# Kernel tuning notes

Measured on AMD Instinct MI355X. Metric: run time of the kernel, lower is better.

The kernel has to match this reference:

```python
import jax, jax.numpy as jnp
import numpy as np

B, N, H = 8, 512, 256
D2 = H // 2          # per-direction hidden = attention proj = 128
VOCAB, EMB = 100, 256
DIN0 = EMB + 3


def _sru_pp_layer(x, pad, Wq, Wk, Wv, Wu, vf, vr, bf, br):
    # x: (L, Bt, din); pad: (L, Bt) bool, True = padded position
    L, Bt, _ = x.shape
    d2 = Wu.shape[1] // 8
    q = x @ Wq                                   # (L,Bt,proj) attention projection
    k = q @ Wk
    v = q @ Wv
    scale = 1.0 / jnp.sqrt(jnp.asarray(q.shape[-1], q.dtype))
    scores = jnp.einsum('lbp,mbp->blm', q, k) * scale
    scores = jnp.where(pad.T[:, None, :], -1e9, scores)
    a = jnp.einsum('blm,mbp->lbp', jax.nn.softmax(scores, axis=-1), v) + q
    U = (a @ Wu).reshape(L, Bt, 2, 4, d2)        # 2 directions x 4 matrices

    def run_dir(Ud, padd, vf_d, vr_d, bf_d, br_d):
        def step(c, inp):
            u, p = inp                            # u: (Bt,4,d2), p: (Bt,)
            f = jax.nn.sigmoid(u[:, 1] + vf_d * c + bf_d)
            r = jax.nn.sigmoid(u[:, 2] + vr_d * c + br_d)
            c_new = f * c + (1.0 - f) * u[:, 0]
            c_new = jnp.where(p[:, None], c, c_new)
            h = jnp.where(p[:, None], 0.0, r * c_new + (1.0 - r) * u[:, 3])
            return c_new, h
        c0 = jnp.zeros((Bt, d2), x.dtype)
        _, hs = jax.lax.scan(step, c0, (Ud, padd))
        return hs

    hf = run_dir(U[:, :, 0], pad, vf[0], vr[0], bf[0], br[0])
    hb = run_dir(U[::-1, :, 1], pad[::-1], vf[1], vr[1], bf[1], br[1])[::-1]
    return jnp.concatenate([hf, hb], axis=-1)     # (L,Bt,2*d2)


def _forward(noisy_seqs, noisy_cords, mask, emb, params):
    Bb, Nn = noisy_seqs.shape
    X = noisy_cords[:, :, 1]                      # CA coordinates (B,N,3)
    m3 = mask[..., None]
    center = (X * m3).sum(1) / m3.sum(1)
    Xc = X - center[:, None] * m3
    C = jnp.einsum('bni,bnj->bij', Xc, Xc)        # (B,3,3) covariance
    _, V = jnp.linalg.eigh(jax.lax.stop_gradient(C))
    ops = jnp.asarray([[i, j, k] for i in (-1, 1) for j in (-1, 1) for k in (-1, 1)], X.dtype)
    F_ops = ops[None, :, None, :] * V[:, None]    # (B,8,3,3) sign-flipped frames
    hX = jnp.einsum('boji,bpj->bopi', F_ops, Xc).reshape(Bb * 8, Nn, 3)
    seq = jnp.where(noisy_seqs < 0, 82, noisy_seqs)
    hS = jnp.broadcast_to(emb[seq][:, None], (Bb, 8, Nn, emb.shape[1])).reshape(Bb * 8, Nn, -1)
    h = jnp.swapaxes(jnp.concatenate([hX, hS], -1), 0, 1)   # (N, B*8, EMB+3)
    pad = jnp.broadcast_to((mask == 0.0)[:, None], (Bb, 8, Nn)).reshape(Bb * 8, Nn).T
    for p in params:
        h = _sru_pp_layer(h, pad, *p)
    return jnp.swapaxes(h, 0, 1).reshape(Bb, 8, Nn, -1).mean(1)


def setup_inputs():
    key = jax.random.key(0)
    ks = [jax.random.fold_in(key, i) for i in range(32)]
    inp = {
        'noisy_seqs': jax.random.randint(ks[0], (B, N), 0, VOCAB, dtype=jnp.int32),
        'noisy_cords': jax.random.normal(ks[1], (B, N, 4, 3), jnp.float32),
        'mask': jnp.ones((B, N), jnp.float32),
        'emb': 0.02 * jax.random.normal(ks[2], (VOCAB, EMB), jnp.float32),
    }
    i = 3
    for l, din in enumerate([DIN0, H]):
        inp[f'Wq{l}'] = jax.random.normal(ks[i], (din, D2), jnp.float32) / np.sqrt(din); i += 1
        inp[f'Wk{l}'] = jax.random.normal(ks[i], (D2, D2), jnp.float32) / np.sqrt(D2); i += 1
        inp[f'Wv{l}'] = jax.random.normal(ks[i], (D2, D2), jnp.float32) / np.sqrt(D2); i += 1
        inp[f'Wu{l}'] = jax.random.normal(ks[i], (D2, 8 * D2), jnp.float32) / np.sqrt(D2); i += 1
        inp[f'vf{l}'] = 0.1 * jax.random.normal(ks[i], (2, D2), jnp.float32); i += 1
        inp[f'vr{l}'] = 0.1 * jax.random.normal(ks[i], (2, D2), jnp.float32); i += 1
        inp[f'bf{l}'] = jnp.zeros((2, D2), jnp.float32)
        inp[f'br{l}'] = jnp.zeros((2, D2), jnp.float32)
    return inp


def reference(noisy_seqs, noisy_cords, mask, emb,
              Wq0, Wk0, Wv0, Wu0, vf0, vr0, bf0, br0,
              Wq1, Wk1, Wv1, Wu1, vf1, vr1, bf1, br1):
    params = [(Wq0, Wk0, Wv0, Wu0, vf0, vr0, bf0, br0),
              (Wq1, Wk1, Wv1, Wu1, vf1, vr1, bf1, br1)]
    return _forward(noisy_seqs, noisy_cords, mask, emb, params)
```

## Files before the change

### kernel.cpp

```cpp
#include <hip/hip_runtime.h>
#include <hip/hip_bf16.h>
#include <math.h>

#define L_    512
#define F_    64
#define M_    (F_*L_)
#define D2_   128
#define H_    256
#define LOG2E_ 1.4426950408889634f

typedef unsigned short u16;
typedef __attribute__((ext_vector_type(8))) short s16x8;
typedef __attribute__((ext_vector_type(4))) float f32x4;

__device__ inline u16 bf_hi(float x) {
  union { float f; unsigned u; } v; v.f = x;
  unsigned r = v.u + 0x7fffu + ((v.u >> 16) & 1u);
  return (u16)(r >> 16);
}
__device__ inline float bf_to_f(u16 h) {
  union { float f; unsigned u; } v; v.u = ((unsigned)h) << 16; return v.f;
}
__device__ inline void split2(float x, u16& h, u16& l) {
  h = bf_hi(x);
  l = bf_hi(x - bf_to_f(h));
}
__device__ inline float exp2_fast(float x) {
#if __has_builtin(__builtin_amdgcn_exp2f)
  return __builtin_amdgcn_exp2f(x);
#else
  return __expf(x * 0.6931471805599453f);
#endif
}
__device__ inline float rcp_fast(float x) {
#if __has_builtin(__builtin_amdgcn_rcpf)
  return __builtin_amdgcn_rcpf(x);
#else
  return 1.f/x;
#endif
}

#define RSPLIT_A 18432
#define RSPLIT_B 26624

__global__ void geom_kernel(const float* __restrict__ cords, const float* __restrict__ mask,
                            float* __restrict__ misc) {
  int b = blockIdx.x;
  int t = threadIdx.x;
  __shared__ float red[4][256];
  float sx=0.f, sy=0.f, sz=0.f, sm=0.f;
  for (int l = t; l < 512; l += 256) {
    float m = mask[b*512 + l];
    const float* X = cords + ((size_t)(b*512 + l)*4 + 1)*3;
    sx += X[0]*m; sy += X[1]*m; sz += X[2]*m; sm += m;
  }
  red[0][t]=sx; red[1][t]=sy; red[2][t]=sz; red[3][t]=sm;
  __syncthreads();
  for (int off=128; off>0; off>>=1) {
    if (t < off) { red[0][t]+=red[0][t+off]; red[1][t]+=red[1][t+off];
                   red[2][t]+=red[2][t+off]; red[3][t]+=red[3][t+off]; }
    __syncthreads();
  }
  float inv = 1.f/red[3][0];
  float cx = red[0][0]*inv, cy = red[1][0]*inv, cz = red[2][0]*inv;
  __syncthreads();
  __shared__ float red6[6][256];
  float c00=0,c01=0,c02=0,c11=0,c12=0,c22=0;
  for (int l = t; l < 512; l += 256) {
    float m = mask[b*512+l];
    const float* X = cords + ((size_t)(b*512+l)*4 + 1)*3;
    float x = X[0]-cx*m, y = X[1]-cy*m, z = X[2]-cz*m;
    c00+=x*x; c01+=x*y; c02+=x*z; c11+=y*y; c12+=y*z; c22+=z*z;
  }
  red6[0][t]=c00; red6[1][t]=c01; red6[2][t]=c02;
  red6[3][t]=c11; red6[4][t]=c12; red6[5][t]=c22;
  __syncthreads();
  for (int off=128; off>0; off>>=1) {
    if (t < off) for (int j=0;j<6;j++) red6[j][t]+=red6[j][t+off];
    __syncthreads();
  }
  if (t == 0) {
    double A[3][3], V[3][3];
    A[0][0]=red6[0][0]; A[0][1]=A[1][0]=red6[1][0]; A[0][2]=A[2][0]=red6[2][0];
    A[1][1]=red6[3][0]; A[1][2]=A[2][1]=red6[4][0]; A[2][2]=red6[5][0];
    for (int j=0;j<3;j++) for (int i=0;i<3;i++) V[j][i] = (i==j)?1.0:0.0;
    for (int sweep=0; sweep<10; ++sweep) {
      for (int p=0;p<2;p++) for (int q=p+1;q<3;q++) {
        double apq = A[p][q];
        if (fabs(apq) < 1e-18) continue;
        double app = A[p][p], aqq = A[q][q];
        double tau = (aqq - app) / (2.0*apq);
        double tt = (tau >= 0.0) ? 1.0/(tau + sqrt(1.0+tau*tau))
                                 : 1.0/(tau - sqrt(1.0+tau*tau));
        double cc = 1.0/sqrt(1.0+tt*tt), ss = tt*cc;
        A[p][p] = app - tt*apq;
        A[q][q] = aqq + tt*apq;
        A[p][q] = A[q][p] = 0.0;
        int r = 3 - p - q;
        double arp = A[r][p], arq = A[r][q];
        A[r][p] = A[p][r] = cc*arp - ss*arq;
        A[r][q] = A[q][r] = ss*arp + cc*arq;
        for (int rr2=0; rr2<3; ++rr2) {
          double vrp = V[rr2][p], vrq = V[rr2][q];
          V[rr2][p] = cc*vrp - ss*vrq;
          V[rr2][q] = ss*vrp + cc*vrq;
        }
      }
    }
    double w[3] = {A[0][0], A[1][1], A[2][2]};
    int idx[3] = {0,1,2};
    for (int i=0;i<2;i++) for (int j=0;j<2-i;j++)
      if (w[idx[j]] > w[idx[j+1]]) { int tmp=idx[j]; idx[j]=idx[j+1]; idx[j+1]=tmp; }
    for (int jj=0;jj<3;jj++) for (int ii=0;ii<3;ii++)
      misc[b*12 + jj*3 + ii] = (float)V[jj][idx[ii]];
    misc[b*12+9]=cx; misc[b*12+10]=cy; misc[b*12+11]=cz;
  }
}

__global__ void build_h0(const int* __restrict__ seqs, const float* __restrict__ cords,
                         const float* __restrict__ mask, const float* __restrict__ emb,
                         const float* __restrict__ misc,
                         u16* __restrict__ h0h, u16* __restrict__ h0l) {
  int t = threadIdx.x;
  int r = blockIdx.x*4 + (t >> 6);
  int lane = t & 63;
  int f = r >> 9, l = r & 511;
  int b = f >> 3, o = f & 7;
  u16* rh = h0h + (size_t)r * 288;
  u16* rl = h0l + (size_t)r * 288;
  if (lane == 0) {
    float m = mask[b*512 + l];
    const float* X = cords + ((size_t)(b*512 + l)*4 + 1)*3;
    const float* mb = misc + b*12;
    float x = X[0]-mb[9]*m, y = X[1]-mb[10]*m, z = X[2]-mb[11]*m;
    #pragma unroll
    for (int i=0;i<3;i++) {
      float sgn = ((o >> (2-i)) & 1) ? 1.f : -1.f;
      float val = sgn * (mb[0+i]*x + mb[3+i]*y + mb[6+i]*z);
      u16 h,lo; split2(val,h,lo); rh[i]=h; rl[i]=lo;
    }
  }
  if (lane < 29) { rh[259+lane] = 0; rl[259+lane] = 0; }
  int s = seqs[b*512 + l];
  if (s < 0) s = 82;
  const float4 e4 = *((const float4*)(emb + (size_t)s*256) + lane);
  float ev[4] = {e4.x, e4.y, e4.z, e4.w};
  #pragma unroll
  for (int i=0;i<4;i++) {
    u16 h,lo; split2(ev[i],h,lo);
    rh[3 + lane*4 + i] = h; rl[3 + lane*4 + i] = lo;
  }
}

__global__ void prep_wqkv_mul(const float* __restrict__ Wq, const float* __restrict__ Wk,
                              const float* __restrict__ Wv,
                              float* __restrict__ wqk, float* __restrict__ wqv) {
  int k = blockIdx.x;
  int y = blockIdx.y;
  int t = threadIdx.x;
  __shared__ float row[128];
  row[t] = Wq[(size_t)k*128 + t];
  __syncthreads();
  const float* W2 = y ? Wv : Wk;
  float acc = 0.f;
  for (int j = 0; j < 128; j++) acc += row[j] * W2[(size_t)j*128 + t];
  (y ? wqv : wqk)[(size_t)k*128 + t] = acc;
}

__global__ void prep_wT3(const float* __restrict__ Wq, const float* __restrict__ wqk,
                         const float* __restrict__ wqv,
                         u16* __restrict__ Th, u16* __restrict__ Tl,
                         int K, int KP) {
  int y = blockIdx.y;
  int n = blockIdx.x;
  const float* W = (y==0) ? Wq : (y==1) ? wqk : wqv;
  int row = y*128 + n;
  for (int k = threadIdx.x; k < KP; k += 128) {
    float x = (k < K) ? W[(size_t)k*128 + n] : 0.f;
    u16 h,l; split2(x,h,l);
    Th[(size_t)row*KP + k] = h; Tl[(size_t)row*KP + k] = l;
  }
}

__global__ void prep_wu(const float* __restrict__ Wu, u16* __restrict__ Th, u16* __restrict__ Tl,
                        const float* __restrict__ bfv, const float* __restrict__ brv,
                        float* __restrict__ nbf, float* __restrict__ nbr) {
  int n = blockIdx.x;
  int dir = blockIdx.y;
  int k = threadIdx.x;
  int d = n >> 2, g = n & 3;
  float x = Wu[(size_t)k*1024 + (dir*4+g)*128 + d];
  if (g == 1 || g == 2) x *= -LOG2E_;
  u16 h,l; split2(x,h,l);
  size_t o = ((size_t)dir*512 + n)*128 + k;
  Th[o]=h; Tl[o]=l;
  if (n == 0) {
    nbf[dir*128 + k] = bfv[dir*128 + k] * (-LOG2E_);
    nbr[dir*128 + k] = brv[dir*128 + k] * (-LOG2E_);
  }
}

__global__ __launch_bounds__(256) void gemm_qkv(
    const u16* __restrict__ Ah, const u16* __restrict__ Al,
    const u16* __restrict__ Bh, const u16* __restrict__ Bl,
    int KP,
    u16* __restrict__ Ch, u16* __restrict__ Cl,
    u16* __restrict__ Dh, u16* __restrict__ Dl,
    u16* __restrict__ Eh, u16* __restrict__ El)
{
  __shared__ u16 As[2][64][40];
  __shared__ u16 Bs[2][128][40];
  const int t = threadIdx.x;
  const int bm = blockIdx.x * 64, bn = blockIdx.y * 128;
  const int lane = t & 63;
  const int w = t >> 6;
  const int fr = lane & 15, g = lane >> 4;

  f32x4 acc[4][2] = {};

  for (int k0 = 0; k0 < KP; k0 += 32) {
    {
      int m = t >> 2, sub = t & 3;
      const size_t ga = (size_t)(bm + m)*KP + k0 + sub*8;
      *(int4*)&As[0][m][sub*8] = *(const int4*)(Ah + ga);
      *(int4*)&As[1][m][sub*8] = *(const int4*)(Al + ga);
    }
    #pragma unroll
    for (int cc = 0; cc < 2; cc++) {
      int c = t + cc*256;
      int m = c >> 2, sub = c & 3;
      const size_t gb = (size_t)(bn + m)*KP + k0 + sub*8;
      *(int4*)&Bs[0][m][sub*8] = *(const int4*)(Bh + gb);
      *(int4*)&Bs[1][m][sub*8] = *(const int4*)(Bl + gb);
    }
    __syncthreads();
    s16x8 af[4][2], bfr[2][2];
    #pragma unroll
    for (int i = 0; i < 4; i++) {
      af[i][0] = *(const s16x8*)&As[0][i*16 + fr][g*8];
      af[i][1] = *(const s16x8*)&As[1][i*16 + fr][g*8];
    }
    #pragma unroll
    for (int j = 0; j < 2; j++) {
      bfr[j][0] = *(const s16x8*)&Bs[0][w*32 + j*16 + fr][g*8];
      bfr[j][1] = *(const s16x8*)&Bs[1][w*32 + j*16 + fr][g*8];
    }
    #pragma unroll
    for (int mi = 0; mi < 4; mi++)
      #pragma unroll
      for (int nj = 0; nj < 2; nj++)
        acc[mi][nj] = __builtin_amdgcn_mfma_f32_16x16x32_bf16(af[mi][0], bfr[nj][0], acc[mi][nj], 0,0,0);
    #pragma unroll
    for (int mi = 0; mi < 4; mi++)
      #pragma unroll
      for (int nj = 0; nj < 2; nj++)
        acc[mi][nj] = __builtin_amdgcn_mfma_f32_16x16x32_bf16(af[mi][0], bfr[nj][1], acc[mi][nj], 0,0,0);
    #pragma unroll
    for (int mi = 0; mi < 4; mi++)
      #pragma unroll
      for (int nj = 0; nj < 2; nj++)
        acc[mi][nj] = __builtin_amdgcn_mfma_f32_16x16x32_bf16(af[mi][1], bfr[nj][0], acc[mi][nj], 0,0,0);
    __syncthreads();
  }

  #pragma unroll
  for (int mi = 0; mi < 4; mi++) {
    #pragma unroll
    for (int nj = 0; nj < 2; nj++) {
      #pragma unroll
      for (int rg = 0; rg < 4; rg++) {
        int r = bm + mi*16 + g*4 + rg;
        int n = bn + w*32 + nj*16 + fr;
        float val = acc[mi][nj][rg];
        u16 h,l; split2(val,h,l);
        if (blockIdx.y == 0) {
          size_t o = (size_t)r*128 + n;
          Ch[o]=h; Cl[o]=l;
        } else if (blockIdx.y == 1) {
          size_t o = (size_t)r*128 + (n - 128);
          Dh[o]=h; Dl[o]=l;
        } else {
          size_t o = ((size_t)(r >> 9)*128 + (n - 256))*512 + (r & 511);
          Eh[o]=h; El[o]=l;
        }
      }
    }
  }
}

template<int EPI>
__global__ __launch_bounds__(256) void gemm_bb(
    const u16* __restrict__ Ah, const u16* __restrict__ Al,
    const u16* __restrict__ Bh, const u16* __restrict__ Bl,
    int KP, int lda, int ldb,
    long aBatch, long bBatch, long cBatch,
    u16* __restrict__ Ch, u16* __restrict__ Cl, int ldc,
    float* __restrict__ F0, float* __restrict__ F1, float* __restrict__ F2,
    float* __restrict__ F3, float* __restrict__ F4, float* __restrict__ F5,
    const u16* __restrict__ rh, const u16* __restrict__ rl,
    const float* __restrict__ maskp, const float* __restrict__ nbf,
    const float* __restrict__ nbr, float scale, int dirOff)
{
  __shared__ u16 As[2][128][40];
  __shared__ u16 Bs[2][128][40];
  __shared__ float epsM[128];
  __shared__ float epsA[128];
  const int t = threadIdx.x;
  const int z = blockIdx.z;
  const int bm = blockIdx.x * 128, bn = blockIdx.y * 128;
  Ah += (size_t)z * aBatch; Al += (size_t)z * aBatch;
  Bh += (size_t)z * bBatch; Bl += (size_t)z * bBatch;

  const int lane = t & 63;
  const int w = t >> 6, wr = w >> 1, wc = w & 1;
  const int fr = lane & 15, g = lane >> 4;

  const bool isD1 = (bn >= 512);
  const int dirU = dirOff + (isD1 ? 1 : 0);
  if (EPI == 4) {
    if (t < 128) {
      int r = bm + t;
      epsM[t] = maskp[(r >> 12)*512 + (r & 511)];
      int nl = (bn + t) & 511;
      int dd = nl >> 2, gg2 = nl & 3;
      epsA[t] = (gg2==1) ? nbf[dirU*128 + dd] : (gg2==2) ? nbr[dirU*128 + dd] : 0.f;
    }
  }

  f32x4 acc[4][4] = {};

  for (int k0 = 0; k0 < KP; k0 += 32) {
    #pragma unroll
    for (int cc = 0; cc < 2; cc++) {
      int c = t + cc*256;
      int m = c >> 2, sub = c & 3;
      const size_t ga = (size_t)(bm + m)*lda + k0 + sub*8;
      const size_t gb = (size_t)(bn + m)*ldb + k0 + sub*8;
      *(int4*)&As[0][m][sub*8] = *(const int4*)(Ah + ga);
      *(int4*)&As[1][m][sub*8] = *(const int4*)(Al + ga);
      *(int4*)&Bs[0][m][sub*8] = *(const int4*)(Bh + gb);
      *(int4*)&Bs[1][m][sub*8] = *(const int4*)(Bl + gb);
    }
    __syncthreads();
    s16x8 af[4][2], bfr[4][2];
    #pragma unroll
    for (int i = 0; i < 4; i++) {
      af[i][0]  = *(const s16x8*)&As[0][wr*64 + i*16 + fr][g*8];
      af[i][1]  = *(const s16x8*)&As[1][wr*64 + i*16 + fr][g*8];
      bfr[i][0] = *(const s16x8*)&Bs[0][wc*64 + i*16 + fr][g*8];
      bfr[i][1] = *(const s16x8*)&Bs[1][wc*64 + i*16 + fr][g*8];
    }
    #pragma unroll
    for (int mi = 0; mi < 4; mi++)
      #pragma unroll
      for (int nj = 0; nj < 4; nj++)
        acc[mi][nj] = __builtin_amdgcn_mfma_f32_16x16x32_bf16(af[mi][0], bfr[nj][0], acc[mi][nj], 0,0,0);
    #pragma unroll
    for (int mi = 0; mi < 4; mi++)
      #pragma unroll
      for (int nj = 0; nj < 4; nj++)
        acc[mi][nj] = __builtin_amdgcn_mfma_f32_16x16x32_bf16(af[mi][0], bfr[nj][1], acc[mi][nj], 0,0,0);
    #pragma unroll
    for (int mi = 0; mi < 4; mi++)
      #pragma unroll
      for (int nj = 0; nj < 4; nj++)
        acc[mi][nj] = __builtin_amdgcn_mfma_f32_16x16x32_bf16(af[mi][1], bfr[nj][0], acc[mi][nj], 0,0,0);
    __syncthreads();
  }

  const int rbase = bm + wr*64, nbase = bn + wc*64;
  float* tA = isD1 ? F3 : F0;
  float* tB = isD1 ? F4 : F1;
  float* tC = isD1 ? F5 : F2;
  const int gg = fr & 3;
  const float ovr = (gg==1) ? -16384.f : (gg==2) ? 16384.f : 0.f;

  #pragma unroll
  for (int mi = 0; mi < 4; mi++) {
    #pragma unroll
    for (int nj = 0; nj < 4; nj++) {
      #pragma unroll
      for (int rg = 0; rg < 4; rg++) {
        int r = rbase + mi*16 + g*4 + rg;
        int n = nbase + nj*16 + fr;
        float val = acc[mi][nj][rg];
        if (EPI == 2) {
          float vv = val * scale;
          if (maskp[(z>>3)*512 + n] == 0.f) vv = -1e9f;
          F0[(size_t)z*cBatch + (size_t)r*ldc + n] = vv;
        } else if (EPI == 3) {
          size_t o = (size_t)z*cBatch + (size_t)r*ldc + n;
          float vv = val + (bf_to_f(rh[o]) + bf_to_f(rl[o]));
          u16 h,l; split2(vv,h,l);
          Ch[o]=h; Cl[o]=l;
        } else if (EPI == 4) {
          int nloc = (n & 511);
          val += epsA[n - bn];
          if (epsM[r - bm] == 0.f) val = ovr;
          float* Up;
          if (r < RSPLIT_A)      Up = tA + (size_t)r*512;
          else if (r < RSPLIT_B) Up = tB + (size_t)(r - RSPLIT_A)*512;
          else                   Up = tC + (size_t)(r - RSPLIT_B)*512;
          Up[nloc] = val;
        }
      }
    }
  }
}

__global__ __launch_bounds__(256) void attn_flash(
    const u16* __restrict__ qh, const u16* __restrict__ ql,
    const u16* __restrict__ kh, const u16* __restrict__ kl,
    const u16* __restrict__ vTh, const u16* __restrict__ vTl,
    const float* __restrict__ maskp,
    u16* __restrict__ ah, u16* __restrict__ al, float scale)
{
  __shared__ u16 As[2][64][36];
  __shared__ u16 Bs[2][128][36];
  __shared__ u16 Ps[2][64][68];
  __shared__ float rmaxL[2][64];
  __shared__ float rsumL[2][64];
  __shared__ float mskt[64];
  const int t = threadIdx.x;
  const int bid = blockIdx.x;
  const int xcd  = bid & 7;
  const int rest = bid >> 3;
  const int tile = rest & 7;
  const int f    = (rest >> 3)*8 + xcd;
  const int bq = f >> 3;
  const int bm = tile * 64;
  const size_t qrow0 = (size_t)f*512 + bm;
  const int lane = t & 63;
  const int w = t >> 6, wr = w >> 1, wc = w & 1;
  const int fr = lane & 15, g = lane >> 4;
  const int m_ = t >> 2, sub_ = t & 3;

  float mrun[2][4], srun[2][4];
  #pragma unroll
  for (int mi=0;mi<2;mi++)
    #pragma unroll
    for (int rg=0;rg<4;rg++) { mrun[mi][rg] = -3e38f; srun[mi][rg] = 0.f; }
  f32x4 Oacc[2][4] = {};

  for (int kt = 0; kt < 8; ++kt) {
    if (t < 64) mskt[t] = maskp[bq*512 + kt*64 + t];
    f32x4 Sacc[2][2] = {};
    #pragma unroll
    for (int k0 = 0; k0 < 4; ++k0) {
      {
        const size_t ga = (qrow0 + m_)*128 + k0*32 + sub_*8;
        const size_t gb = ((size_t)f*512 + kt*64 + m_)*128 + k0*32 + sub_*8;
        *(int4*)&As[0][m_][sub_*8] = *(const int4*)(qh + ga);
        *(int4*)&As[1][m_][sub_*8] = *(const int4*)(ql + ga);
        *(int4*)&Bs[0][m_][sub_*8] = *(const int4*)(kh + gb);
        *(int4*)&Bs[1][m_][sub_*8] = *(const int4*)(kl + gb);
      }
      __syncthreads();
      s16x8 af[2][2], bf2[2][2];
      #pragma unroll
      for (int i = 0; i < 2; i++) {
        af[i][0]  = *(const s16x8*)&As[0][wr*32 + i*16 + fr][g*8];
        af[i][1]  = *(const s16x8*)&As[1][wr*32 + i*16 + fr][g*8];
        bf2[i][0] = *(const s16x8*)&Bs[0][wc*32 + i*16 + fr][g*8];
        bf2[i][1] = *(const s16x8*)&Bs[1][wc*32 + i*16 + fr][g*8];
      }
      #pragma unroll
      for (int mi = 0; mi < 2; mi++)
        #pragma unroll
        for (int nj = 0; nj < 2; nj++)
          Sacc[mi][nj] = __builtin_amdgcn_mfma_f32_16x16x32_bf16(af[mi][0], bf2[nj][0], Sacc[mi][nj], 0,0,0);
      #pragma unroll
      for (int mi = 0; mi < 2; mi++)
        #pragma unroll
        for (int nj = 0; nj < 2; nj++)
          Sacc[mi][nj] = __builtin_amdgcn_mfma_f32_16x16x32_bf16(af[mi][0], bf2[nj][1], Sacc[mi][nj], 0,0,0);
      #pragma unroll
      for (int mi = 0; mi < 2; mi++)
        #pragma unroll
        for (int nj = 0; nj < 2; nj++)
          Sacc[mi][nj] = __builtin_amdgcn_mfma_f32_16x16x32_bf16(af[mi][1], bf2[nj][0], Sacc[mi][nj], 0,0,0);
      __syncthreads();
    }
    float mkv[2];
    mkv[0] = mskt[wc*32 + fr];
    mkv[1] = mskt[wc*32 + 16 + fr];
    float rm[2][4];
    #pragma unroll
    for (int mi=0;mi<2;mi++)
      #pragma unroll
      for (int rg=0;rg<4;rg++) rm[mi][rg] = -3e38f;
    #pragma unroll
    for (int mi=0;mi<2;mi++)
      #pragma unroll
      for (int nj=0;nj<2;nj++)
        #pragma unroll
        for (int rg=0;rg<4;rg++) {
          float sv = Sacc[mi][nj][rg]*scale;
          sv = (mkv[nj]==0.f) ? -1e9f : sv;
          Sacc[mi][nj][rg] = sv;
          rm[mi][rg] = fmaxf(rm[mi][rg], sv);
        }
    #pragma unroll
    for (int off=1; off<16; off<<=1)
      #pragma unroll
      for (int mi=0;mi<2;mi++)
        #pragma unroll
        for (int rg=0;rg<4;rg++) rm[mi][rg] = fmaxf(rm[mi][rg], __shfl_xor(rm[mi][rg], off));
    if (fr == 0) {
      #pragma unroll
      for (int mi=0;mi<2;mi++)
        #pragma unroll
        for (int rg=0;rg<4;rg++) rmaxL[wc][wr*32 + mi*16 + g*4 + rg] = rm[mi][rg];
    }
    __syncthreads();
    float alpha[2][4], rs[2][4];
    #pragma unroll
    for (int mi=0;mi<2;mi++)
      #pragma unroll
      for (int rg=0;rg<4;rg++) {
        int rl_ = wr*32 + mi*16 + g*4 + rg;
        float tmax = fmaxf(rmaxL[0][rl_], rmaxL[1][rl_]);
        float mn = fmaxf(mrun[mi][rg], tmax);
        alpha[mi][rg] = exp2_fast((mrun[mi][rg] - mn)*LOG2E_);
        mrun[mi][rg] = mn;
        rs[mi][rg] = 0.f;
      }
    #pragma unroll
    for (int mi=0;mi<2;mi++)
      #pragma unroll
      for (int nj=0;nj<2;nj++)
        #pragma unroll
        for (int rg=0;rg<4;rg++) {
          float p = exp2_fast((Sacc[mi][nj][rg] - mrun[mi][rg])*LOG2E_);
          rs[mi][rg] += p;
          u16 h,l; split2(p,h,l);
          int rl_ = wr*32 + mi*16 + g*4 + rg;
          int cl_ = wc*32 + nj*16 + fr;
          Ps[0][rl_][cl_] = h;
          Ps[1][rl_][cl_] = l;
        }
    #pragma unroll
    for (int off=1; off<16; off<<=1)
      #pragma unroll
      for (int mi=0;mi<2;mi++)
        #pragma unroll
        for (int rg=0;rg<4;rg++) rs[mi][rg] += __shfl_xor(rs[mi][rg], off);
    if (fr == 0) {
      #pragma unroll
      for (int mi=0;mi<2;mi++)
        #pragma unroll
        for (int rg=0;rg<4;rg++) rsumL[wc][wr*32 + mi*16 + g*4 + rg] = rs[mi][rg];
    }
    #pragma unroll
    for (int mi=0;mi<2;mi++)
      #pragma unroll
      for (int nj=0;nj<4;nj++)
        #pragma unroll
        for (int rg=0;rg<4;rg++) Oacc[mi][nj][rg] *= alpha[mi][rg];
    __syncthreads();
    #pragma unroll
    for (int mi=0;mi<2;mi++)
      #pragma unroll
      for (int rg=0;rg<4;rg++) {
        int rl_ = wr*32 + mi*16 + g*4 + rg;
        srun[mi][rg] = srun[mi][rg]*alpha[mi][rg] + rsumL[0][rl_] + rsumL[1][rl_];
      }
    #pragma unroll
    for (int k0 = 0; k0 < 2; ++k0) {
      #pragma unroll
      for (int cc = 0; cc < 2; cc++) {
        int c = t + cc*256;
        int mv = c >> 2, sb = c & 3;
        const size_t gv = ((size_t)f*128 + mv)*512 + kt*64 + k0*32 + sb*8;
        *(int4*)&Bs[0][mv][sb*8] = *(const int4*)(vTh + gv);
        *(int4*)&Bs[1][mv][sb*8] = *(const int4*)(vTl + gv);
      }
      __syncthreads();
      s16x8 pa[2][2], pb[4][2];
      #pragma unroll
      for (int i = 0; i < 2; i++) {
        pa[i][0] = *(const s16x8*)&Ps[0][wr*32 + i*16 + fr][k0*32 + g*8];
        pa[i][1] = *(const s16x8*)&Ps[1][wr*32 + i*16 + fr][k0*32 + g*8];
      }
      #pragma unroll
      for (int j = 0; j < 4; j++) {
        pb[j][0] = *(const s16x8*)&Bs[0][wc*64 + j*16 + fr][g*8];
        pb[j][1] = *(const s16x8*)&Bs[1][wc*64 + j*16 + fr][g*8];
      }
      #pragma unroll
      for (int mi = 0; mi < 2; mi++)
        #pragma unroll
        for (int nj = 0; nj < 4; nj++)
          Oacc[mi][nj] = __builtin_amdgcn_mfma_f32_16x16x32_bf16(pa[mi][0], pb[nj][0], Oacc[mi][nj], 0,0,0);
      #pragma unroll
      for (int mi = 0; mi < 2; mi++)
        #pragma unroll
        for (int nj = 0; nj < 4; nj++)
          Oacc[mi][nj] = __builtin_amdgcn_mfma_f32_16x16x32_bf16(pa[mi][0], pb[nj][1], Oacc[mi][nj], 0,0,0);
      #pragma unroll
      for (int mi = 0; mi < 2; mi++)
        #pragma unroll
        for (int nj = 0; nj < 4; nj++)
          Oacc[mi][nj] = __builtin_amdgcn_mfma_f32_16x16x32_bf16(pa[mi][1], pb[nj][0], Oacc[mi][nj], 0,0,0);
      __syncthreads();
    }
  }
  float inv[2][4];
  #pragma unroll
  for (int mi=0;mi<2;mi++)
    #pragma unroll
    for (int rg=0;rg<4;rg++) inv[mi][rg] = 1.f / srun[mi][rg];
  #pragma unroll
  for (int mi=0;mi<2;mi++)
    #pragma unroll
    for (int nj=0;nj<4;nj++)
      #pragma unroll
      for (int rg=0;rg<4;rg++) {
        int rl_ = wr*32 + mi*16 + g*4 + rg;
        int cl_ = wc*64 + nj*16 + fr;
        size_t o = (qrow0 + rl_)*128 + cl_;
        float val = Oacc[mi][nj][rg]*inv[mi][rg] + bf_to_f(qh[o]) + bf_to_f(ql[o]);
        u16 h,l; split2(val,h,l);
        ah[o]=h; al[o]=l;
      }
}

__global__ void softmax_split(float* __restrict__ S) {
  size_t row = blockIdx.x;
  float* p = S + row*512;
  u16* ph = (u16*)p;
  u16* pl = ph + 512;
  int t = threadIdx.x;
  float v[8];
  float mx = -1e30f;
  #pragma unroll
  for (int i=0;i<8;i++) { v[i] = p[t + i*64]; mx = fmaxf(mx, v[i]); }
  #pragma unroll
  for (int off=32; off>0; off>>=1) mx = fmaxf(mx, __shfl_xor(mx, off));
  float sum = 0.f;
  #pragma unroll
  for (int i=0;i<8;i++) { v[i] = __expf(v[i]-mx); sum += v[i]; }
  #pragma unroll
  for (int off=32; off>0; off>>=1) sum += __shfl_xor(sum, off);
  float invs = 1.f/sum;
  #pragma unroll
  for (int i=0;i<8;i++) {
    float x = v[i]*invs;
    u16 h,l; split2(x,h,l);
    ph[t + i*64] = h; pl[t + i*64] = l;
  }
}

#define CH_ 8
#define LOADC(buf, ch) do { \
  int _c = (ch); \
  _Pragma("unroll") \
  for (int s = 0; s < CH_; s++) { \
    int l = (_c*CH_ + s) ^ lxor; \
    buf[s] = *(const float4*)(Ubase + (size_t)l*512); \
  } \
  __builtin_amdgcn_sched_barrier(0); \
} while(0)

#define COMPC(buf, ch) do { \
  int _c = (ch); \
  _Pragma("unroll") \
  for (int s = 0; s < CH_; s++) { \
    int l = (_c*CH_ + s) ^ lxor; \
    float4 u = buf[s]; \
    float ef = exp2_fast(fmaf(nvfd, cstate, u.y)); \
    float fg = rcp_fast(1.f + ef); \
    float er = exp2_fast(fmaf(nvrd, cstate, u.z)); \
    float rg = rcp_fast(1.f + er); \
    float cn = fmaf(fg, cstate - u.x, u.x); \
    float h  = fmaf(rg, cn - u.w, u.w); \
    cstate = cn; \
    if (PAIRS) { \
      u16 sh_, sl_; split2(h, sh_, sl_); \
      hpph[(size_t)l*256] = sh_; \
      hppl[(size_t)l*256] = sl_; \
    } else { \
      h32p[(size_t)l*256] = h; \
    } \
  } \
  __builtin_amdgcn_sched_barrier(0); \
} while(0)

template<int PAIRS>
__global__ __launch_bounds__(64, 1) void sru_scan(
                          const float* __restrict__ ua0, const float* __restrict__ ub0,
                          const float* __restrict__ uc0,
                          const float* __restrict__ ua1, const float* __restrict__ ub1,
                          const float* __restrict__ uc1,
                          const float* __restrict__ vf, const float* __restrict__ vr,
                          u16* __restrict__ hph, u16* __restrict__ hpl,
                          float* __restrict__ h32, int dirArg) {
  const int blk = blockIdx.x;
  const int f = blk >> 1;
  const int hh = blk & 1;
  const int dir = dirArg + blockIdx.y;
  const int t = threadIdx.x;
  const int lxor = dir ? 511 : 0;
  const int d = hh*64 + t;
  const float nvfd = vf[dir*128 + d] * (-LOG2E_);
  const float nvrd = vr[dir*128 + d] * (-LOG2E_);
  const size_t fbase = (size_t)f * 512;
  const float* ua = dir ? ua1 : ua0;
  const float* ub = dir ? ub1 : ub0;
  const float* uc = dir ? uc1 : uc0;
  const float* Uf;
  if (f < 36)      Uf = ua + (size_t)f*(512*512);
  else if (f < 52) Uf = ub + (size_t)(f-36)*(512*512);
  else             Uf = uc + (size_t)(f-52)*(512*512);
  const float* Ubase = Uf + d*4;
  u16* hpph = hph + fbase*256 + (size_t)dir*128 + d;
  u16* hppl = hpl + fbase*256 + (size_t)dir*128 + d;
  float* h32p = h32 + fbase*256 + (size_t)dir*128 + d;

  float4 b0[CH_], b1[CH_], b2[CH_], b3[CH_];
  LOADC(b0, 0); LOADC(b1, 1);
  float cstate = 0.f;
  #pragma unroll 1
  for (int q4 = 0; q4 < 15; q4++) {
    const int base = q4*4;
    LOADC(b2, base+2);
    COMPC(b0, base);
    LOADC(b3, base+3);
    COMPC(b1, base+1);
    LOADC(b0, base+4);
    COMPC(b2, base+2);
    LOADC(b1, base+5);
    COMPC(b3, base+3);
  }
  LOADC(b2, 62);
  COMPC(b0, 60);
  LOADC(b3, 63);
  COMPC(b1, 61);
  COMPC(b2, 62);
  COMPC(b3, 63);
}

__global__ void mean_kernel(const float* __restrict__ h2, float* __restrict__ out) {
  int i = blockIdx.x*256 + threadIdx.x;
  int row = i >> 6;
  int c4  = i & 63;
  int b = row >> 9, l = row & 511;
  float ax=0.f, ay=0.f, az=0.f, aw=0.f;
  #pragma unroll
  for (int o=0;o<8;o++) {
    const float4* p = (const float4*)(h2 + ((size_t)((b*8+o)*512 + l))*256) + c4;
    float4 e = *p;
    ax += e.x; ay += e.y; az += e.z; aw += e.w;
  }
  float4 r; r.x = ax*0.125f; r.y = ay*0.125f; r.z = az*0.125f; r.w = aw*0.125f;
  ((float4*)out)[i] = r;
}

extern "C" void kernel_launch(void* const* d_in, const int* in_sizes, int n_in,
                              void* d_out, int out_size, void* d_ws, size_t ws_size,
                              hipStream_t stream) {
  const int*   seqs  = (const int*)d_in[0];
  const float* cords = (const float*)d_in[1];
  const float* mask  = (const float*)d_in[2];
  const float* emb   = (const float*)d_in[3];
  const float* Wq[2] = {(const float*)d_in[4],  (const float*)d_in[12]};
  const float* Wk[2] = {(const float*)d_in[5],  (const float*)d_in[13]};
  const float* Wv[2] = {(const float*)d_in[6],  (const float*)d_in[14]};
  const float* Wu[2] = {(const float*)d_in[7],  (const float*)d_in[15]};
  const float* vf[2] = {(const float*)d_in[8],  (const float*)d_in[16]};
  const float* vr[2] = {(const float*)d_in[9],  (const float*)d_in[17]};
  const float* bfp[2]= {(const float*)d_in[10], (const float*)d_in[18]};
  const float* brp[2]= {(const float*)d_in[11], (const float*)d_in[19]};

  const size_t H0_B = 2*(size_t)M_*288*2;
  const size_t Q_B  = 2*(size_t)M_*128*2;
  const size_t S_B  = (size_t)M_*512*4;
  const size_t HP_B = 2*(size_t)M_*256*2;
  const size_t W_B  = (size_t)(2*1024*128)*2 + 2*256*4;

  const size_t NEED_MERGED = 4096 + H0_B + 3*Q_B + S_B + HP_B + W_B;
  const bool merged = (ws_size >= NEED_MERGED);

  char* base = (char*)d_ws;
  float* misc = (float*)base;
  u16* h0p_h = (u16*)(base + 4096);
  u16* h0p_l = h0p_h + (size_t)M_*288;
  u16* q_h   = (u16*)(base + 4096 + H0_B);
  u16* q_l   = q_h + (size_t)M_*128;
  u16* k_h   = (u16*)(base + 4096 + H0_B + Q_B);
  u16* k_l   = k_h + (size_t)M_*128;

  u16 *vT_h, *vT_l, *a_h, *a_l;
  float *S, *tail_w;
  u16 *hp_h, *hp_l;
  float *U1A, *U1B, *U1C;
  if (merged) {
    vT_h = (u16*)(base + 4096 + H0_B + 2*Q_B);
    vT_l = vT_h + (size_t)M_*128;
    S    = (float*)(base + 4096 + H0_B + 3*Q_B);
    hp_h = (u16*)((char*)S + S_B);
    hp_l = hp_h + (size_t)M_*256;
    tail_w = (float*)((char*)hp_h + HP_B);
    U1A = (float*)h0p_h;
    U1B = (float*)q_h;
    U1C = (float*)vT_h;
    a_h = hp_h;
    a_l = hp_h + (size_t)M_*128;
  } else {
    S    = (float*)(base + 4096 + H0_B + 2*Q_B);
    hp_h = (u16*)((char*)S + S_B);
    hp_l = hp_h + (size_t)M_*256;
    vT_h = hp_h; vT_l = hp_l;
    tail_w = (float*)((char*)hp_h + HP_B);
    U1A = S; U1B = S + (size_t)RSPLIT_A*512; U1C = S + (size_t)RSPLIT_B*512;
    a_h = k_h; a_l = k_l;
  }
  float* U0A = S;
  float* U0B = S + (size_t)RSPLIT_A*512;
  float* U0C = S + (size_t)RSPLIT_B*512;
  float* h32 = (float*)hp_h;

  float* wqk32 = S;
  float* wqv32 = wqk32 + 288*128;
  u16*   wT3h  = (u16*)(wqv32 + 288*128);
  u16*   wT3l  = wT3h + 384*288;
  u16* wuT_h = (u16*)tail_w;
  u16* wuT_l = wuT_h + 1024*128;
  float* nbf = (float*)(wuT_l + 1024*128);
  float* nbr = nbf + 256;

  geom_kernel<<<8, 256, 0, stream>>>(cords, mask, misc);
  build_h0<<<M_/4, 256, 0, stream>>>(seqs, cords, mask, emb, misc, h0p_h, h0p_l);

  const float scale = 0.08838834764831845f;
  for (int layer = 0; layer < 2; ++layer) {
    const u16* Ah_in = layer ? hp_h : h0p_h;
    const u16* Al_in = layer ? hp_l : h0p_l;
    const int  Kq    = layer ? 256 : 259;
    const int  KPq   = layer ? 256 : 288;

    prep_wqkv_mul<<<dim3(Kq,2), 128, 0, stream>>>(Wq[layer], Wk[layer], Wv[layer], wqk32, wqv32);
    prep_wT3<<<dim3(128,3), 128, 0, stream>>>(Wq[layer], wqk32, wqv32, wT3h, wT3l, Kq, KPq);
    prep_wu<<<dim3(512,2), 128, 0, stream>>>(Wu[layer], wuT_h, wuT_l, bfp[layer], brp[layer], nbf, nbr);

    gemm_qkv<<<dim3(512,3), 256, 0, stream>>>(Ah_in, Al_in, wT3h, wT3l,
        KPq, q_h, q_l, k_h, k_l, vT_h, vT_l);

    if (merged) {
      attn_flash<<<512, 256, 0, stream>>>(q_h, q_l, k_h, k_l, vT_h, vT_l,
          mask, a_h, a_l, scale);
    } else {
      gemm_bb<2><<<dim3(4,4,64), 256, 0, stream>>>(q_h, q_l, k_h, k_l,
          128, 128, 128, 512*128, 512*128, 512*512, nullptr,nullptr, 512,
          S,nullptr,nullptr,nullptr,nullptr,nullptr,
          nullptr,nullptr, mask,nullptr,nullptr, scale, 0);
      softmax_split<<<M_, 64, 0, stream>>>(S);
      gemm_bb<3><<<dim3(4,1,64), 256, 0, stream>>>((const u16*)S, (const u16*)S + 512, vT_h, vT_l,
          512, 1024, 512, 512*1024, 128*512, 512*128, a_h, a_l, 128,
          nullptr,nullptr,nullptr,nullptr,nullptr,nullptr,
          q_h, q_l, nullptr,nullptr,nullptr, 0.f, 0);
    }

    if (merged) {
      gemm_bb<4><<<dim3(256,8,1), 256, 0, stream>>>(a_h, a_l, wuT_h, wuT_l,
          128, 128, 128, 0,0,0, nullptr,nullptr, 512,
          U0A,U0B,U0C, U1A,U1B,U1C,
          nullptr,nullptr, mask, nbf, nbr, 0.f, 0);
      if (layer == 0)
        sru_scan<1><<<dim3(128,2), 64, 0, stream>>>(U0A,U0B,U0C, U1A,U1B,U1C,
            vf[layer], vr[layer], hp_h, hp_l, h32, 0);
      else
        sru_scan<0><<<dim3(128,2), 64, 0, stream>>>(U0A,U0B,U0C, U1A,U1B,U1C,
            vf[layer], vr[layer], hp_h, hp_l, h32, 0);
    } else {
      for (int dir = 0; dir < 2; ++dir) {
        gemm_bb<4><<<dim3(256,4,1), 256, 0, stream>>>(a_h, a_l,
            wuT_h + (size_t)dir*512*128, wuT_l + (size_t)dir*512*128,
            128, 128, 128, 0,0,0, nullptr,nullptr, 512,
            U0A,U0B,U0C, U0A,U0B,U0C,
            nullptr,nullptr, mask, nbf, nbr, 0.f, dir);
        if (layer == 0)
          sru_scan<1><<<dim3(128,1), 64, 0, stream>>>(U0A,U0B,U0C, U0A,U0B,U0C,
              vf[layer], vr[layer], hp_h, hp_l, h32, dir);
        else
          sru_scan<0><<<dim3(128,1), 64, 0, stream>>>(U0A,U0B,U0C, U0A,U0B,U0C,
              vf[layer], vr[layer], hp_h, hp_l, h32, dir);
      }
    }
  }
  mean_kernel<<<1024, 256, 0, stream>>>(h32, (float*)d_out);
}
```

Measured before the change: 442.1 us.

## Halve flash-attention query tile to 32 rows and double block count

The flash attention kernel now handles 32 query rows per block instead of 64, so it launches 1024 blocks instead of 512. The four waves are re-split along the key/value column dimension, and the shared buffers are merged into one union buffer. The aim is more parallelism and better CU occupancy on the MI355X. In exchange, every K and V tile is loaded from global memory twice as often, and the row max/sum reduction now spans four waves.

```diff
diff --git a/kernel.cpp b/kernel.cpp
--- a/kernel.cpp
+++ b/kernel.cpp
@@ -415,91 +415,81 @@
     const float* __restrict__ maskp,
     u16* __restrict__ ah, u16* __restrict__ al, float scale)
 {
-  __shared__ u16 As[2][64][36];
-  __shared__ u16 Bs[2][128][36];
-  __shared__ u16 Ps[2][64][68];
-  __shared__ float rmaxL[2][64];
-  __shared__ float rsumL[2][64];
+  __shared__ __align__(16) u16 UB[9216];
+  __shared__ u16 Ps[2][32][68];
+  __shared__ float rmaxL[4][32];
+  __shared__ float rsumL[4][32];
   __shared__ float mskt[64];
   const int t = threadIdx.x;
   const int bid = blockIdx.x;
   const int xcd  = bid & 7;
   const int rest = bid >> 3;
-  const int tile = rest & 7;
-  const int f    = (rest >> 3)*8 + xcd;
+  const int tile = rest & 15;
+  const int f    = (rest >> 4)*8 + xcd;
   const int bq = f >> 3;
-  const int bm = tile * 64;
+  const int bm = tile * 32;
   const size_t qrow0 = (size_t)f*512 + bm;
   const int lane = t & 63;
-  const int w = t >> 6, wr = w >> 1, wc = w & 1;
+  const int w = t >> 6;
   const int fr = lane & 15, g = lane >> 4;
-  const int m_ = t >> 2, sub_ = t & 3;
 
   float mrun[2][4], srun[2][4];
   #pragma unroll
   for (int mi=0;mi<2;mi++)
     #pragma unroll
     for (int rg=0;rg<4;rg++) { mrun[mi][rg] = -3e38f; srun[mi][rg] = 0.f; }
-  f32x4 Oacc[2][4] = {};
+  f32x4 Oacc[2][2] = {};
 
   for (int kt = 0; kt < 8; ++kt) {
     if (t < 64) mskt[t] = maskp[bq*512 + kt*64 + t];
-    f32x4 Sacc[2][2] = {};
+    f32x4 Sacc[2] = {};
     #pragma unroll
     for (int k0 = 0; k0 < 4; ++k0) {
       {
-        const size_t ga = (qrow0 + m_)*128 + k0*32 + sub_*8;
-        const size_t gb = ((size_t)f*512 + kt*64 + m_)*128 + k0*32 + sub_*8;
-        *(int4*)&As[0][m_][sub_*8] = *(const int4*)(qh + ga);
-        *(int4*)&As[1][m_][sub_*8] = *(const int4*)(ql + ga);
-        *(int4*)&Bs[0][m_][sub_*8] = *(const int4*)(kh + gb);
-        *(int4*)&Bs[1][m_][sub_*8] = *(const int4*)(kl + gb);
+        int pl = t >> 7, id = t & 127, row = id >> 2, sub = id & 3;
+        const u16* src = pl ? ql : qh;
+        *(int4*)&UB[pl*1152 + row*36 + sub*8] =
+          *(const int4*)(src + (qrow0 + row)*128 + k0*32 + sub*8);
+      }
+      #pragma unroll
+      for (int cc = 0; cc < 2; cc++) {
+        int c = cc*256 + t;
+        int pl = c >> 8, id = c & 255, row = id >> 2, sub = id & 3;
+        const u16* src = pl ? kl : kh;
+        *(int4*)&UB[2304 + pl*2304 + row*36 + sub*8] =
+          *(const int4*)(src + ((size_t)f*512 + kt*64 + row)*128 + k0*32 + sub*8);
       }
       __syncthreads();
-      s16x8 af[2][2], bf2[2][2];
+      s16x8 af[2][2], bf2[2];
       #pragma unroll
       for (int i = 0; i < 2; i++) {
-        af[i][0]  = *(const s16x8*)&As[0][wr*32 + i*16 + fr][g*8];
-        af[i][1]  = *(const s16x8*)&As[1][wr*32 + i*16 + fr][g*8];
-        bf2[i][0] = *(const s16x8*)&Bs[0][wc*32 + i*16 + fr][g*8];
-        bf2[i][1] = *(const s16x8*)&Bs[1][wc*32 + i*16 + fr][g*8];
-      }
+        af[i][0] = *(const s16x8*)&UB[        (i*16 + fr)*36 + g*8];
+        af[i][1] = *(const s16x8*)&UB[1152 + (i*16 + fr)*36 + g*8];
+      }
+      bf2[0] = *(const s16x8*)&UB[2304 +        (w*16 + fr)*36 + g*8];
+      bf2[1] = *(const s16x8*)&UB[2304 + 2304 + (w*16 + fr)*36 + g*8];
       #pragma unroll
       for (int mi = 0; mi < 2; mi++)
-        #pragma unroll
-        for (int nj = 0; nj < 2; nj++)
-          Sacc[mi][nj] = __builtin_amdgcn_mfma_f32_16x16x32_bf16(af[mi][0], bf2[nj][0], Sacc[mi][nj], 0,0,0);
+        Sacc[mi] = __builtin_amdgcn_mfma_f32_16x16x32_bf16(af[mi][0], bf2[0], Sacc[mi], 0,0,0);
       #pragma unroll
       for (int mi = 0; mi < 2; mi++)
-        #pragma unroll
-        for (int nj = 0; nj < 2; nj++)
-          Sacc[mi][nj] = __builtin_amdgcn_mfma_f32_16x16x32_bf16(af[mi][0], bf2[nj][1], Sacc[mi][nj], 0,0,0);
+        Sacc[mi] = __builtin_amdgcn_mfma_f32_16x16x32_bf16(af[mi][0], bf2[1], Sacc[mi], 0,0,0);
       #pragma unroll
       for (int mi = 0; mi < 2; mi++)
-        #pragma unroll
-        for (int nj = 0; nj < 2; nj++)
-          Sacc[mi][nj] = __builtin_amdgcn_mfma_f32_16x16x32_bf16(af[mi][1], bf2[nj][0], Sacc[mi][nj], 0,0,0);
+        Sacc[mi] = __builtin_amdgcn_mfma_f32_16x16x32_bf16(af[mi][1], bf2[0], Sacc[mi], 0,0,0);
       __syncthreads();
     }
-    float mkv[2];
-    mkv[0] = mskt[wc*32 + fr];
-    mkv[1] = mskt[wc*32 + 16 + fr];
+    const float mkv = mskt[w*16 + fr];
     float rm[2][4];
     #pragma unroll
     for (int mi=0;mi<2;mi++)
       #pragma unroll
-      for (int rg=0;rg<4;rg++) rm[mi][rg] = -3e38f;
-    #pragma unroll
-    for (int mi=0;mi<2;mi++)
-      #pragma unroll
-      for (int nj=0;nj<2;nj++)
-        #pragma unroll
-        for (int rg=0;rg<4;rg++) {
-          float sv = Sacc[mi][nj][rg]*scale;
-          sv = (mkv[nj]==0.f) ? -1e9f : sv;
-          Sacc[mi][nj][rg] = sv;
-          rm[mi][rg] = fmaxf(rm[mi][rg], sv);
-        }
+      for (int rg=0;rg<4;rg++) {
+        float sv = Sacc[mi][rg]*scale;
+        sv = (mkv==0.f) ? -1e9f : sv;
+        Sacc[mi][rg] = sv;
+        rm[mi][rg] = sv;
+      }
     #pragma unroll
     for (int off=1; off<16; off<<=1)
       #pragma unroll
@@ -510,7 +500,7 @@
       #pragma unroll
       for (int mi=0;mi<2;mi++)
         #pragma unroll
-        for (int rg=0;rg<4;rg++) rmaxL[wc][wr*32 + mi*16 + g*4 + rg] = rm[mi][rg];
+        for (int rg=0;rg<4;rg++) rmaxL[w][mi*16 + g*4 + rg] = rm[mi][rg];
     }
     __syncthreads();
     float alpha[2][4], rs[2][4];
@@ -518,8 +508,9 @@
     for (int mi=0;mi<2;mi++)
       #pragma unroll
       for (int rg=0;rg<4;rg++) {
-        int rl_ = wr*32 + mi*16 + g*4 + rg;
-        float tmax = fmaxf(rmaxL[0][rl_], rmaxL[1][rl_]);
+        int rl_ = mi*16 + g*4 + rg;
+        float tmax = fmaxf(fmaxf(rmaxL[0][rl_], rmaxL[1][rl_]),
+                           fmaxf(rmaxL[2][rl_], rmaxL[3][rl_]));
         float mn = fmaxf(mrun[mi][rg], tmax);
         alpha[mi][rg] = exp2_fast((mrun[mi][rg] - mn)*LOG2E_);
         mrun[mi][rg] = mn;
@@ -528,17 +519,15 @@
     #pragma unroll
     for (int mi=0;mi<2;mi++)
       #pragma unroll
-      for (int nj=0;nj<2;nj++)
-        #pragma unroll
-        for (int rg=0;rg<4;rg++) {
-          float p = exp2_fast((Sacc[mi][nj][rg] - mrun[mi][rg])*LOG2E_);
-          rs[mi][rg] += p;
-          u16 h,l; split2(p,h,l);
-          int rl_ = wr*32 + mi*16 + g*4 + rg;
-          int cl_ = wc*32 + nj*16 + fr;
-          Ps[0][rl_][cl_] = h;
-          Ps[1][rl_][cl_] = l;
-        }
+      for (int rg=0;rg<4;rg++) {
+        float p = exp2_fast((Sacc[mi][rg] - mrun[mi][rg])*LOG2E_);
+        rs[mi][rg] += p;
+        u16 h,l; split2(p,h,l);
+        int rl_ = mi*16 + g*4 + rg;
+        int cl_ = w*16 + fr;
+        Ps[0][rl_][cl_] = h;
+        Ps[1][rl_][cl_] = l;
+      }
     #pragma unroll
     for (int off=1; off<16; off<<=1)
       #pragma unroll
@@ -549,12 +538,12 @@
       #pragma unroll
       for (int mi=0;mi<2;mi++)
         #pragma unroll
-        for (int rg=0;rg<4;rg++) rsumL[wc][wr*32 + mi*16 + g*4 + rg] = rs[mi][rg];
+        for (int rg=0;rg<4;rg++) rsumL[w][mi*16 + g*4 + rg] = rs[mi][rg];
     }
     #pragma unroll
     for (int mi=0;mi<2;mi++)
       #pragma unroll
-      for (int nj=0;nj<4;nj++)
+      for (int nj=0;nj<2;nj++)
         #pragma unroll
         for (int rg=0;rg<4;rg++) Oacc[mi][nj][rg] *= alpha[mi][rg];
     __syncthreads();
@@ -562,45 +551,46 @@
     for (int mi=0;mi<2;mi++)
       #pragma unroll
       for (int rg=0;rg<4;rg++) {
-        int rl_ = wr*32 + mi*16 + g*4 + rg;
-        srun[mi][rg] = srun[mi][rg]*alpha[mi][rg] + rsumL[0][rl_] + rsumL[1][rl_];
+        int rl_ = mi*16 + g*4 + rg;
+        srun[mi][rg] = srun[mi][rg]*alpha[mi][rg]
+                     + rsumL[0][rl_] + rsumL[1][rl_] + rsumL[2][rl_] + rsumL[3][rl_];
       }
     #pragma unroll
     for (int k0 = 0; k0 < 2; ++k0) {
       #pragma unroll
-      for (int cc = 0; cc < 2; cc++) {
-        int c = t + cc*256;
-        int mv = c >> 2, sb = c & 3;
-        const size_t gv = ((size_t)f*128 + mv)*512 + kt*64 + k0*32 + sb*8;
-        *(int4*)&Bs[0][mv][sb*8] = *(const int4*)(vTh + gv);
-        *(int4*)&Bs[1][mv][sb*8] = *(const int4*)(vTl + gv);
+      for (int cc = 0; cc < 4; cc++) {
+        int c = cc*256 + t;
+        int pl = c >> 9, id = c & 511, d = id >> 2, sub = id & 3;
+        const u16* src = pl ? vTl : vTh;
+        *(int4*)&UB[pl*4608 + d*36 + sub*8] =
+          *(const int4*)(src + ((size_t)f*128 + d)*512 + kt*64 + k0*32 + sub*8);
       }
       __syncthreads();
-      s16x8 pa[2][2], pb[4][2];
+      s16x8 pa[2][2], pb[2][2];
       #pragma unroll
       for (int i = 0; i < 2; i++) {
-        pa[i][0] = *(const s16x8*)&Ps[0][wr*32 + i*16 + fr][k0*32 + g*8];
-        pa[i][1] = *(const s16x8*)&Ps[1][wr*32 + i*16 + fr][k0*32 + g*8];
-      }
-      #pragma unroll
-      for (int j = 0; j < 4; j++) {
-        pb[j][0] = *(const s16x8*)&Bs[0][wc*64 + j*16 + fr][g*8];
-        pb[j][1] = *(const s16x8*)&Bs[1][wc*64 + j*16 + fr][g*8];
+        pa[i][0] = *(const s16x8*)&Ps[0][i*16 + fr][k0*32 + g*8];
+        pa[i][1] = *(const s16x8*)&Ps[1][i*16 + fr][k0*32 + g*8];
+      }
+      #pragma unroll
+      for (int j = 0; j < 2; j++) {
+        pb[j][0] = *(const s16x8*)&UB[        (w*32 + j*16 + fr)*36 + g*8];
+        pb[j][1] = *(const s16x8*)&UB[4608 + (w*32 + j*16 + fr)*36 + g*8];
       }
       #pragma unroll
       for (int mi = 0; mi < 2; mi++)
         #pragma unroll
-        for (int nj = 0; nj < 4; nj++)
+        for (int nj = 0; nj < 2; nj++)
           Oacc[mi][nj] = __builtin_amdgcn_mfma_f32_16x16x32_bf16(pa[mi][0], pb[nj][0], Oacc[mi][nj], 0,0,0);
       #pragma unroll
       for (int mi = 0; mi < 2; mi++)
         #pragma unroll
-        for (int nj = 0; nj < 4; nj++)
+        for (int nj = 0; nj < 2; nj++)
           Oacc[mi][nj] = __builtin_amdgcn_mfma_f32_16x16x32_bf16(pa[mi][0], pb[nj][1], Oacc[mi][nj], 0,0,0);
       #pragma unroll
       for (int mi = 0; mi < 2; mi++)
         #pragma unroll
-        for (int nj = 0; nj < 4; nj++)
+        for (int nj = 0; nj < 2; nj++)
           Oacc[mi][nj] = __builtin_amdgcn_mfma_f32_16x16x32_bf16(pa[mi][1], pb[nj][0], Oacc[mi][nj], 0,0,0);
       __syncthreads();
     }
@@ -613,11 +603,11 @@
   #pragma unroll
   for (int mi=0;mi<2;mi++)
     #pragma unroll
-    for (int nj=0;nj<4;nj++)
+    for (int nj=0;nj<2;nj++)
       #pragma unroll
       for (int rg=0;rg<4;rg++) {
-        int rl_ = wr*32 + mi*16 + g*4 + rg;
-        int cl_ = wc*64 + nj*16 + fr;
+        int rl_ = mi*16 + g*4 + rg;
+        int cl_ = w*32 + nj*16 + fr;
         size_t o = (qrow0 + rl_)*128 + cl_;
         float val = Oacc[mi][nj][rg]*inv[mi][rg] + bf_to_f(qh[o]) + bf_to_f(ql[o]);
         u16 h,l; split2(val,h,l);
@@ -847,7 +837,7 @@
         KPq, q_h, q_l, k_h, k_l, vT_h, vT_l);
 
     if (merged) {
-      attn_flash<<<512, 256, 0, stream>>>(q_h, q_l, k_h, k_l, vT_h, vT_l,
+      attn_flash<<<1024, 256, 0, stream>>>(q_h, q_l, k_h, k_l, vT_h, vT_l,
           mask, a_h, a_l, scale);
     } else {
       gemm_bb<2><<<dim3(4,4,64), 256, 0, stream>>>(q_h, q_l, k_h, k_l,
```

After: 523.6 us. 1.18x slower.
